# Kernel optimization log

Measured on AMD Instinct MI355X. Metric: run time of the kernel, lower is better.

## Reference

```python
import jax, jax.numpy as jnp
import numpy as np

N, E, G = 50000, 1600000, 64
N_SPECIES, D_ATTR, D, N_RBF = 16, 16, 32, 8
CUTOFF = 5.0
SCALE, SHIFT = 1.0, 0.0


def setup_inputs() -> dict:
    key = jax.random.key(0)
    ks = jax.random.split(key, 20)

    def w(k, shape):
        fan_in = shape[-2] if len(shape) > 1 else shape[-1]
        return jax.random.normal(k, shape, dtype=jnp.float32) / np.sqrt(fan_in)

    return {
        "x": jax.random.randint(ks[0], (N, 1), 0, N_SPECIES),
        "pos": 3.0 * jax.random.normal(ks[1], (N, 3), dtype=jnp.float32),
        "edge_index": jax.random.randint(ks[2], (2, E), 0, N),
        "period_vec": 0.1 * jax.random.normal(ks[3], (E, 3), dtype=jnp.float32),
        "batch": jnp.sort(jax.random.randint(ks[4], (N,), 0, G)),
        "W_elem": w(ks[5], (N_SPECIES, D_ATTR)),
        "W0": w(ks[6], (D_ATTR, D)),
        "b0": jnp.zeros((D,), jnp.float32),
        "Wr1": w(ks[7], (3, N_RBF, D)),
        "br1": jnp.zeros((3, D), jnp.float32),
        "Wr2": w(ks[8], (3, D, D)),
        "Wmsg": w(ks[9], (3, D, D)),
        "Wattr": w(ks[10], (3, D_ATTR, D)),
        "Wself": w(ks[11], (3, D, D)),
        "bconv": jnp.zeros((3, D), jnp.float32),
        "wsh": w(ks[12], (3, 4)),
        "Wp1": w(ks[13], (D, 16)),
        "bp1": jnp.zeros((16,), jnp.float32),
        "Wp2": w(ks[14], (16, 1)),
        "bp2": jnp.zeros((1,), jnp.float32),
    }


def reference(x, pos, edge_index, period_vec, batch, W_elem, W0, b0, Wr1, br1,
              Wr2, Wmsg, Wattr, Wself, bconv, wsh, Wp1, bp1, Wp2, bp2):
    src, dst = edge_index[0], edge_index[1]

    # node_attr_layer: species embedding (gather), then first_atom_embed linear
    x_attr = W_elem[x[:, 0]]                              # [N, D_ATTR]
    h = x_attr @ W0 + b0                                  # [N, D]

    # edge_attr_layer: PBC edge vectors, lengths, l<=1 spherical harmonics
    edge_vec = pos[dst] - pos[src] + period_vec           # [E, 3]
    edge_len = jnp.linalg.norm(edge_vec, axis=-1, keepdims=True)  # [E, 1]
    unit = edge_vec / (edge_len + 1e-9)
    edge_sh = jnp.concatenate([jnp.ones_like(edge_len), unit], axis=-1)  # [E, 4]

    # edge_embedding_layer: Gaussian radial basis of edge lengths
    centers = jnp.linspace(0.0, CUTOFF, N_RBF, dtype=pos.dtype)
    gamma = jnp.asarray((N_RBF / CUTOFF) ** 2, pos.dtype)
    rbf = jnp.exp(-gamma * (edge_len - centers) ** 2)     # [E, N_RBF]

    # 3 conv layers: gather -> per-edge transform -> scatter-sum -> node update
    for i in range(3):
        rw = jax.nn.relu(rbf @ Wr1[i] + br1[i]) @ Wr2[i]  # [E, D] radial MLP
        sh_w = edge_sh @ wsh[i]                           # [E] sh mixing
        msg = (h[src] @ Wmsg[i]) * rw * sh_w[:, None]     # [E, D]
        agg = jax.ops.segment_sum(msg, dst, num_segments=N)  # [N, D]
        h = jax.nn.silu(agg + x_attr @ Wattr[i] + h @ Wself[i] + bconv[i])

    # post_conv layers
    h = jax.nn.silu(h @ Wp1 + bp1)                        # [N, 16]
    h = (h @ Wp2 + bp2)[:, 0]                             # [N] (squeeze)

    # scatter-sum pooling over graphs + affine energy scaling
    e = jax.ops.segment_sum(h, batch, num_segments=G)     # [G]
    return (e * SCALE + SHIFT)[:, None]                   # [G, 1]
```

## Files before the change

### kernel.cpp

```cpp
#include <hip/hip_runtime.h>
#include <hip/hip_fp16.h>
#include <math.h>

constexpr int N_NODES  = 50000;
constexpr int N_EDGES  = 1600000;
constexpr int G_GRAPHS = 64;
constexpr int D        = 32;
constexpr int D_ATTR   = 16;
constexpr int N_RBF    = 8;

constexpr int   TBL      = 8192;
constexpr int   TBL_ROWS = TBL + 1;
constexpr float LMAX     = 10.0f;

constexpr int BUCKET = 80;

constexpr int NT     = 64;
constexpr int NTILES = (N_NODES + NT - 1) / NT;
constexpr int TCAP   = 2432;
constexpr int STHREADS = 512;
constexpr int NBLK1    = 1024;
constexpr int EPB      = (N_EDGES + NBLK1 - 1) / NBLK1;
constexpr int EPV      = (EPB + STHREADS - 1) / STHREADS;

constexpr int NSLOT = NTILES * NT * BUCKET;

typedef unsigned int  uint4v  __attribute__((ext_vector_type(4)));
typedef unsigned int  uint2v  __attribute__((ext_vector_type(2)));

__device__ __forceinline__ float silu(float x) {
    return x / (1.0f + __expf(-x));
}
__device__ __forceinline__ float h2f_bits(unsigned short u) {
    return __half2float(__ushort_as_half(u));
}
__device__ __forceinline__ __half2 h2u(unsigned v) {
    union { unsigned u; __half2 h; } c; c.u = v; return c.h;
}

__device__ __forceinline__ void accum8(uint4v t, uint4v m, float sw, float (&acc)[8]) {
    float2 p0 = __half22float2(__hmul2(h2u(t.x), h2u(m.x)));
    float2 p1 = __half22float2(__hmul2(h2u(t.y), h2u(m.y)));
    float2 p2 = __half22float2(__hmul2(h2u(t.z), h2u(m.z)));
    float2 p3 = __half22float2(__hmul2(h2u(t.w), h2u(m.w)));
    acc[0] = fmaf(p0.x, sw, acc[0]); acc[1] = fmaf(p0.y, sw, acc[1]);
    acc[2] = fmaf(p1.x, sw, acc[2]); acc[3] = fmaf(p1.y, sw, acc[3]);
    acc[4] = fmaf(p2.x, sw, acc[4]); acc[5] = fmaf(p2.y, sw, acc[5]);
    acc[6] = fmaf(p3.x, sw, acc[6]); acc[7] = fmaf(p3.y, sw, acc[7]);
}

__global__ void node_init_kernel(const int* __restrict__ x,
                                 const float* __restrict__ W_elem,
                                 const float* __restrict__ W0,
                                 const float* __restrict__ b0,
                                 const float* __restrict__ Wmsg0,
                                 const float* __restrict__ Wself0,
                                 const float* __restrict__ Wattr,
                                 const float* __restrict__ bconv,
                                 __half* __restrict__ hm0,
                                 float* __restrict__ hs0,
                                 float* __restrict__ xa1,
                                 float* __restrict__ xa2,
                                 float* __restrict__ out) {
    int t = blockIdx.x * blockDim.x + threadIdx.x;
    if (t < G_GRAPHS) out[t] = 0.0f;
    int n = t >> 5, c = t & 31;
    if (n >= N_NODES) return;
    int sp = x[n];
    const float* we = W_elem + sp * D_ATTR;
    float xv = (c < D_ATTR) ? we[c] : 0.0f;
    float acc = b0[c];
#pragma unroll
    for (int a = 0; a < D_ATTR; ++a) acc += we[a] * W0[a * D + c];
    float m = 0.0f, s = 0.0f;
#pragma unroll
    for (int j = 0; j < D; ++j) {
        float hj = __shfl(acc, j, 32);
        m = fmaf(hj, Wmsg0[j * D + c], m);
        s = fmaf(hj, Wself0[j * D + c], s);
    }
    float a0 = bconv[0 * D + c], a1 = bconv[1 * D + c], a2 = bconv[2 * D + c];
#pragma unroll
    for (int j = 0; j < D_ATTR; ++j) {
        float xj = __shfl(xv, j, 32);
        a0 = fmaf(xj, Wattr[0 * D_ATTR * D + j * D + c], a0);
        a1 = fmaf(xj, Wattr[1 * D_ATTR * D + j * D + c], a1);
        a2 = fmaf(xj, Wattr[2 * D_ATTR * D + j * D + c], a2);
    }
    hm0[n * D + c] = __float2half(m);
    hs0[n * D + c] = s + a0;
    xa1[n * D + c] = a1;
    xa2[n * D + c] = a2;
}

__global__ __launch_bounds__(STHREADS, 8) void hist_kernel(const int* __restrict__ eidx,
                                                           int* __restrict__ blk_hist) {
    __shared__ int hist[NTILES];
    int tid = threadIdx.x;
    int e0 = blockIdx.x * EPB;
    int elim = e0 + EPB < N_EDGES ? e0 + EPB : N_EDGES;
    for (int i = tid; i < NTILES; i += STHREADS) hist[i] = 0;
    __syncthreads();
#pragma unroll
    for (int i = 0; i < EPV; ++i) {
        int e = e0 + tid + STHREADS * i;
        if (e < elim) atomicAdd(&hist[eidx[N_EDGES + e] >> 6], 1);
    }
    __syncthreads();
    int* dst = blk_hist + (size_t)blockIdx.x * NTILES;
    for (int t = tid; t < NTILES; t += STHREADS) dst[t] = hist[t];
}

__global__ void scan_kernel(const int* __restrict__ blk_hist,
                            int* __restrict__ blk_base,
                            int* __restrict__ tile_total) {
    int t = blockIdx.x;
    int lane = threadIdx.x;
    int run = 0;
    for (int b0 = 0; b0 < NBLK1; b0 += 64) {
        int b = b0 + lane;
        int v = (b < NBLK1) ? blk_hist[(size_t)b * NTILES + t] : 0;
        int pre = v;
#pragma unroll
        for (int o = 1; o < 64; o <<= 1) {
            int w = __shfl_up(pre, o);
            if (lane >= o) pre += w;
        }
        int excl = pre - v;
        if (b < NBLK1) blk_base[(size_t)b * NTILES + t] = run + excl;
        run += __shfl(pre, 63);
    }
    if (lane == 0) tile_total[t] = run;
}

__global__ __launch_bounds__(STHREADS, 8) void scatter_kernel(const int* __restrict__ eidx,
                                                              const float* __restrict__ pos,
                                                              const float* __restrict__ period,
                                                              const float* __restrict__ wsh,
                                                              const int* __restrict__ blk_base,
                                                              uint4v* __restrict__ bins) {
    __shared__ int hist[NTILES];
    __shared__ int basev[NTILES];
    int tid = threadIdx.x;
    int e0 = blockIdx.x * EPB;
    int elim = e0 + EPB < N_EDGES ? e0 + EPB : N_EDGES;
    const int* bb = blk_base + (size_t)blockIdx.x * NTILES;
    for (int i = tid; i < NTILES; i += STHREADS) {
        hist[i] = 0;
        basev[i] = bb[i];
    }
    __syncthreads();

    int   sarr[EPV], darr[EPV];
    float vx[EPV], vy[EPV], vz[EPV];
#pragma unroll
    for (int i = 0; i < EPV; ++i) {
        int e  = e0 + tid + STHREADS * i;
        int ec = (e < elim) ? e : (elim - 1);
        int s = eidx[ec];
        int d = eidx[N_EDGES + ec];
        sarr[i] = s;
        darr[i] = d;
        vx[i] = pos[d * 3 + 0] - pos[s * 3 + 0] + period[ec * 3 + 0];
        vy[i] = pos[d * 3 + 1] - pos[s * 3 + 1] + period[ec * 3 + 1];
        vz[i] = pos[d * 3 + 2] - pos[s * 3 + 2] + period[ec * 3 + 2];
    }
    asm volatile("" ::
        "v"(vx[0]), "v"(vx[1]), "v"(vx[2]), "v"(vx[3]),
        "v"(vy[0]), "v"(vy[1]), "v"(vy[2]), "v"(vy[3]),
        "v"(vz[0]), "v"(vz[1]), "v"(vz[2]), "v"(vz[3]),
        "v"(sarr[0]), "v"(sarr[1]), "v"(sarr[2]), "v"(sarr[3]),
        "v"(darr[0]), "v"(darr[1]), "v"(darr[2]), "v"(darr[3]));
#pragma unroll
    for (int i = 0; i < EPV; ++i) {
        int e = e0 + tid + STHREADS * i;
        if (e >= elim) continue;
        float len = sqrtf(vx[i] * vx[i] + vy[i] * vy[i] + vz[i] * vz[i]);
        float inv = 1.0f / (len + 1e-9f);
        int idx = (int)fminf(len * ((float)TBL / LMAX) + 0.5f, (float)TBL);
        float sw[3];
#pragma unroll
        for (int l = 0; l < 3; ++l)
            sw[l] = wsh[l * 4 + 0] +
                    (vx[i] * wsh[l * 4 + 1] + vy[i] * wsh[l * 4 + 2] + vz[i] * wsh[l * 4 + 3]) * inv;
        int tile = darr[i] >> 6;
        int rank = atomicAdd(&hist[tile], 1);
        int slot = basev[tile] + rank;
        if (slot < TCAP) {
            unsigned u0 = (unsigned)__half_as_ushort(__float2half(sw[0]));
            unsigned u1 = (unsigned)__half_as_ushort(__float2half(sw[1]));
            unsigned u2 = (unsigned)__half_as_ushort(__float2half(sw[2]));
            uint4v r;
            r.x = (unsigned)sarr[i] | ((unsigned)idx << 16);
            r.y = (unsigned)(darr[i] & (NT - 1));
            r.z = u0 | (u1 << 16);
            r.w = u2;
            bins[(size_t)tile * TCAP + slot] = r;
        }
    }
}

__global__ __launch_bounds__(512, 8) void shuffle_kernel(const uint4v* __restrict__ bins,
                                                         const int* __restrict__ tile_total,
                                                         unsigned int* __restrict__ xs,
                                                         unsigned short* __restrict__ swp,
                                                         int* __restrict__ count) {
    __shared__ int lcur[NT];
    int tile = blockIdx.x;
    int tid = threadIdx.x;
    if (tid < NT) lcur[tid] = 0;
    __syncthreads();
    int cnt = tile_total[tile];
    if (cnt > TCAP) cnt = TCAP;
    const uint4v* base = bins + (size_t)tile * TCAP;
    for (int i = tid; i < cnt; i += 512) {
        uint4v r = __builtin_nontemporal_load(base + i);
        int dl = (int)(r.y & 63u);
        int slot = atomicAdd(&lcur[dl], 1);
        if (slot < BUCKET) {
            size_t g = (size_t)(tile * NT + dl) * BUCKET + slot;
            xs[g] = r.x;
            swp[0 * (size_t)NSLOT + g] = (unsigned short)(r.z & 0xFFFFu);
            swp[1 * (size_t)NSLOT + g] = (unsigned short)(r.z >> 16);
            swp[2 * (size_t)NSLOT + g] = (unsigned short)(r.w & 0xFFFFu);
        }
    }
    __syncthreads();
    if (tid < NT) {
        int node = tile * NT + tid;
        if (node < N_NODES) {
            int c = lcur[tid];
            count[node] = c < BUCKET ? c : BUCKET;
        }
    }
}

__global__ void table_kernel(const float* __restrict__ Wr1,
                             const float* __restrict__ br1,
                             const float* __restrict__ Wr2,
                             __half* __restrict__ table) {
    int t = blockIdx.x * blockDim.x + threadIdx.x;
    if (t >= 3 * TBL_ROWS) return;
    int l = t / TBL_ROWS;
    int idx = t % TBL_ROWS;
    float len = (float)idx * (LMAX / (float)TBL);
    const float gamma = (8.0f / 5.0f) * (8.0f / 5.0f);
    float rbf[N_RBF];
#pragma unroll
    for (int k = 0; k < N_RBF; ++k) {
        float dd = len - (float)k * (5.0f / 7.0f);
        rbf[k] = __expf(-gamma * dd * dd);
    }
    float out[D];
#pragma unroll
    for (int c = 0; c < D; ++c) out[c] = 0.0f;
    for (int j = 0; j < D; ++j) {
        float z = br1[l * D + j];
#pragma unroll
        for (int k = 0; k < N_RBF; ++k) z += rbf[k] * Wr1[l * N_RBF * D + k * D + j];
        z = fmaxf(z, 0.0f);
        const float* w2 = Wr2 + l * D * D + j * D;
#pragma unroll
        for (int c = 0; c < D; ++c) out[c] += z * w2[c];
    }
    __half* dst = table + ((size_t)(l * TBL_ROWS + idx)) * D;
#pragma unroll
    for (int c = 0; c < D; ++c) dst[c] = __float2half(out[c]);
}

template <int LAYER, bool NEXT>
__global__ __launch_bounds__(256, 8) void conv_kernel(const __half* __restrict__ hm,
                            const float* __restrict__ hs,
                            const unsigned int* __restrict__ xs,
                            const unsigned short* __restrict__ swp,
                            const int* __restrict__ count,
                            const __half* __restrict__ table,
                            const float* __restrict__ Wmsg_next,
                            const float* __restrict__ Wself_next,
                            const float* __restrict__ xa_next,
                            __half* __restrict__ hm_out,
                            float* __restrict__ hs_out,
                            float* __restrict__ h_final) {
    __shared__ float sagg[4][2][32];
    int wid = (blockIdx.x * blockDim.x + threadIdx.x) >> 6;
    int na = wid * 2;
    if (na >= N_NODES) return;
    int nb = na + 1;
    int lane = threadIdx.x & 63;
    int w  = (threadIdx.x >> 6) & 3;
    int rg = lane >> 2;
    int cg = lane & 3;

    const uint4v* tab4 = (const uint4v*)(table + (size_t)LAYER * TBL_ROWS * D);
    const uint4v* hm4  = (const uint4v*)hm;
    const unsigned short* swb = swp + (size_t)LAYER * NSLOT;

    int cnta = count[na], cntb = count[nb];
    int bega = na * BUCKET, begb = nb * BUCKET;
    int mx = cnta > cntb ? cnta : cntb;

    float acca[8], accb[8];
#pragma unroll
    for (int j = 0; j < 8; ++j) { acca[j] = 0.0f; accb[j] = 0.0f; }

    for (int k = 0; k < BUCKET; k += 32) {
        int r0 = k + rg, r1 = k + 16 + rg;
        bool va0 = r0 < cnta, va1 = r1 < cnta;
        bool vb0 = r0 < cntb, vb1 = r1 < cntb;
        unsigned ua0 = va0 ? xs[bega + r0] : 0u;
        unsigned ua1 = va1 ? xs[bega + r1] : 0u;
        unsigned ub0 = vb0 ? xs[begb + r0] : 0u;
        unsigned ub1 = vb1 ? xs[begb + r1] : 0u;
        float sa0 = va0 ? h2f_bits(swb[bega + r0]) : 0.0f;
        float sa1 = va1 ? h2f_bits(swb[bega + r1]) : 0.0f;
        float sb0 = vb0 ? h2f_bits(swb[begb + r0]) : 0.0f;
        float sb1 = vb1 ? h2f_bits(swb[begb + r1]) : 0.0f;
        uint4v ta0 = tab4[(size_t)(ua0 >> 16) * 4 + cg];
        uint4v ma0 = hm4[(size_t)(ua0 & 0xFFFFu) * 4 + cg];
        uint4v ta1 = tab4[(size_t)(ua1 >> 16) * 4 + cg];
        uint4v ma1 = hm4[(size_t)(ua1 & 0xFFFFu) * 4 + cg];
        uint4v tb0 = tab4[(size_t)(ub0 >> 16) * 4 + cg];
        uint4v mb0 = hm4[(size_t)(ub0 & 0xFFFFu) * 4 + cg];
        uint4v tb1 = tab4[(size_t)(ub1 >> 16) * 4 + cg];
        uint4v mb1 = hm4[(size_t)(ub1 & 0xFFFFu) * 4 + cg];
        asm volatile("" :: "v"(ta0.x), "v"(ma0.x), "v"(ta1.x), "v"(ma1.x),
                           "v"(tb0.x), "v"(mb0.x), "v"(tb1.x), "v"(mb1.x));
        accum8(ta0, ma0, sa0, acca);
        accum8(ta1, ma1, sa1, acca);
        accum8(tb0, mb0, sb0, accb);
        accum8(tb1, mb1, sb1, accb);
        if (k + 32 >= mx) break;
    }

#pragma unroll
    for (int j = 0; j < 8; ++j) {
        acca[j] += __shfl_xor(acca[j], 4);
        acca[j] += __shfl_xor(acca[j], 8);
        acca[j] += __shfl_xor(acca[j], 16);
        acca[j] += __shfl_xor(acca[j], 32);
        accb[j] += __shfl_xor(accb[j], 4);
        accb[j] += __shfl_xor(accb[j], 8);
        accb[j] += __shfl_xor(accb[j], 16);
        accb[j] += __shfl_xor(accb[j], 32);
    }
    if (rg == 0) {
#pragma unroll
        for (int j = 0; j < 8; ++j) {
            sagg[w][0][cg * 8 + j] = acca[j];
            sagg[w][1][cg * 8 + j] = accb[j];
        }
    }
    __syncthreads();

    int c = lane & 31;
    int hi = lane >> 5;
    int mynode = hi ? nb : na;
    float agg = sagg[w][hi][c];

    float hn = silu(agg + hs[mynode * D + c]);
    if (NEXT) {
        float m = 0.0f, s2 = 0.0f;
#pragma unroll
        for (int j = 0; j < D; ++j) {
            float hj = __shfl(hn, j, 32);
            m  = fmaf(hj, Wmsg_next[j * D + c], m);
            s2 = fmaf(hj, Wself_next[j * D + c], s2);
        }
        hm_out[mynode * D + c] = __float2half(m);
        hs_out[mynode * D + c] = s2 + xa_next[mynode * D + c];
    } else {
        h_final[mynode * D + c] = hn;
    }
}

__global__ void readout_kernel(const float* __restrict__ h,
                               const int* __restrict__ batch,
                               const float* __restrict__ Wp1,
                               const float* __restrict__ bp1,
                               const float* __restrict__ Wp2,
                               const float* __restrict__ bp2,
                               float* __restrict__ out) {
    int n = blockIdx.x * blockDim.x + threadIdx.x;
    float s = 0.0f;
    int b = -1;
    if (n < N_NODES) {
        b = batch[n];
        const float* hrow = h + n * D;
        float acc2 = bp2[0];
#pragma unroll
        for (int m = 0; m < 16; ++m) {
            float a = bp1[m];
#pragma unroll
            for (int j = 0; j < D; ++j) a += hrow[j] * Wp1[j * 16 + m];
            acc2 += silu(a) * Wp2[m];
        }
        s = acc2;
    }
    unsigned long long valid = __ballot(n < N_NODES);
    if (valid == 0ull) return;
    int firstLane = __ffsll(valid) - 1;
    int b0v = __shfl(b, firstLane);
    bool ok = (b == b0v) || (n >= N_NODES);
    if (__all(ok)) {
#pragma unroll
        for (int o = 32; o > 0; o >>= 1) s += __shfl_down(s, o);
        if ((threadIdx.x & 63) == 0) atomicAdd(out + b0v, s);
    } else {
        if (n < N_NODES) atomicAdd(out + b, s);
    }
}

extern "C" void kernel_launch(void* const* d_in, const int* in_sizes, int n_in,
                              void* d_out, int out_size, void* d_ws, size_t ws_size,
                              hipStream_t stream) {
    const int*   x      = (const int*)d_in[0];
    const float* pos    = (const float*)d_in[1];
    const int*   eidx   = (const int*)d_in[2];
    const float* period = (const float*)d_in[3];
    const int*   batch  = (const int*)d_in[4];
    const float* W_elem = (const float*)d_in[5];
    const float* W0     = (const float*)d_in[6];
    const float* b0     = (const float*)d_in[7];
    const float* Wr1    = (const float*)d_in[8];
    const float* br1    = (const float*)d_in[9];
    const float* Wr2    = (const float*)d_in[10];
    const float* Wmsg   = (const float*)d_in[11];
    const float* Wattr  = (const float*)d_in[12];
    const float* Wself  = (const float*)d_in[13];
    const float* bconv  = (const float*)d_in[14];
    const float* wsh    = (const float*)d_in[15];
    const float* Wp1    = (const float*)d_in[16];
    const float* bp1    = (const float*)d_in[17];
    const float* Wp2    = (const float*)d_in[18];
    const float* bp2    = (const float*)d_in[19];

    char* base = (char*)d_ws;
    size_t off = 0;
    auto carve = [&](size_t bytes) -> void* {
        void* p = base + off;
        off = (off + bytes + 255) & ~(size_t)255;
        return p;
    };
    __half*         hm_a        = (__half*)carve((size_t)N_NODES * D * 2);
    __half*         hm_b        = (__half*)carve((size_t)N_NODES * D * 2);
    float*          hs_a        = (float*)carve((size_t)N_NODES * D * 4);
    float*          hs_b        = (float*)carve((size_t)N_NODES * D * 4);
    float*          xa1         = (float*)carve((size_t)N_NODES * D * 4);
    float*          xa2         = (float*)carve((size_t)N_NODES * D * 4);
    float*          h_final     = (float*)carve((size_t)N_NODES * D * 4);
    unsigned int*   xs          = (unsigned int*)carve((size_t)NSLOT * 4);
    unsigned short* swp         = (unsigned short*)carve((size_t)3 * NSLOT * 2);
    uint4v*         bins        = (uint4v*)carve((size_t)NTILES * TCAP * 16);
    int*            blk_hist    = (int*)carve((size_t)NBLK1 * NTILES * 4);
    int*            blk_base    = (int*)carve((size_t)NBLK1 * NTILES * 4);
    int*            tile_total  = (int*)carve((size_t)NTILES * 4);
    int*            count       = (int*)carve((size_t)NTILES * NT * 4);
    __half*         table       = (__half*)carve((size_t)3 * TBL_ROWS * D * 2);
    (void)ws_size; (void)in_sizes; (void)n_in; (void)out_size;

    node_init_kernel<<<(N_NODES * 32 + 255) / 256, 256, 0, stream>>>(
        x, W_elem, W0, b0, Wmsg + 0 * D * D, Wself + 0 * D * D, Wattr, bconv,
        hm_a, hs_a, xa1, xa2, (float*)d_out);
    hist_kernel<<<NBLK1, STHREADS, 0, stream>>>(eidx, blk_hist);
    scan_kernel<<<NTILES, 64, 0, stream>>>(blk_hist, blk_base, tile_total);
    scatter_kernel<<<NBLK1, STHREADS, 0, stream>>>(eidx, pos, period, wsh, blk_base, bins);
    table_kernel<<<(3 * TBL_ROWS + 127) / 128, 128, 0, stream>>>(Wr1, br1, Wr2, table);
    shuffle_kernel<<<NTILES, 512, 0, stream>>>(bins, tile_total, xs, swp, count);

    int cwaves = (N_NODES + 1) / 2;
    int cgrid  = (cwaves * 64 + 255) / 256;
    conv_kernel<0, true><<<cgrid, 256, 0, stream>>>(
        hm_a, hs_a, xs, swp, count, table, Wmsg + 1 * D * D, Wself + 1 * D * D, xa1,
        hm_b, hs_b, nullptr);
    conv_kernel<1, true><<<cgrid, 256, 0, stream>>>(
        hm_b, hs_b, xs, swp, count, table, Wmsg + 2 * D * D, Wself + 2 * D * D, xa2,
        hm_a, hs_a, nullptr);
    conv_kernel<2, false><<<cgrid, 256, 0, stream>>>(
        hm_a, hs_a, xs, swp, count, table, nullptr, nullptr, nullptr,
        nullptr, nullptr, h_final);

    readout_kernel<<<(N_NODES + 255) / 256, 256, 0, stream>>>(h_final, batch, Wp1, bp1, Wp2, bp2,
                                                              (float*)d_out);
}
```

Baseline: 375.3 us.

## Replace tile histogram/scan/shuffle binning with per-node global atomic cursors

Edge bucketing by destination is simplified: instead of a block histogram, a scan, a scatter into tile bins and a shuffle pass, each edge claims a slot in its destination node's fixed bucket with a global atomicAdd on a per-node cursor and writes its packed record there directly. The cursor array is zeroed in the node init kernel and reused as the count, clamped to BUCKET in the conv kernel. This removes three kernels and an intermediate bins buffer, but trades them for contended global atomics and scattered small writes whose slot order is nondeterministic, so the fp summation order varies between runs.

```diff
diff --git a/kernel.cpp b/kernel.cpp
--- a/kernel.cpp
+++ b/kernel.cpp
@@ -14,16 +14,14 @@
 constexpr float LMAX     = 10.0f;
 
 constexpr int BUCKET = 80;
-
 constexpr int NT     = 64;
-constexpr int NTILES = (N_NODES + NT - 1) / NT;
-constexpr int TCAP   = 2432;
+
 constexpr int STHREADS = 512;
 constexpr int NBLK1    = 1024;
 constexpr int EPB      = (N_EDGES + NBLK1 - 1) / NBLK1;
 constexpr int EPV      = (EPB + STHREADS - 1) / STHREADS;
 
-constexpr int NSLOT = NTILES * NT * BUCKET;
+constexpr int NSLOT = N_NODES * BUCKET;
 
 typedef unsigned int  uint4v  __attribute__((ext_vector_type(4)));
 typedef unsigned int  uint2v  __attribute__((ext_vector_type(2)));
@@ -61,9 +59,11 @@
                                  float* __restrict__ hs0,
                                  float* __restrict__ xa1,
                                  float* __restrict__ xa2,
+                                 int* __restrict__ node_cursor,
                                  float* __restrict__ out) {
     int t = blockIdx.x * blockDim.x + threadIdx.x;
     if (t < G_GRAPHS) out[t] = 0.0f;
+    if (t < N_NODES) node_cursor[t] = 0;
     int n = t >> 5, c = t & 31;
     if (n >= N_NODES) return;
     int sp = x[n];
@@ -93,63 +93,16 @@
     xa2[n * D + c] = a2;
 }
 
-__global__ __launch_bounds__(STHREADS, 8) void hist_kernel(const int* __restrict__ eidx,
-                                                           int* __restrict__ blk_hist) {
-    __shared__ int hist[NTILES];
-    int tid = threadIdx.x;
-    int e0 = blockIdx.x * EPB;
-    int elim = e0 + EPB < N_EDGES ? e0 + EPB : N_EDGES;
-    for (int i = tid; i < NTILES; i += STHREADS) hist[i] = 0;
-    __syncthreads();
-#pragma unroll
-    for (int i = 0; i < EPV; ++i) {
-        int e = e0 + tid + STHREADS * i;
-        if (e < elim) atomicAdd(&hist[eidx[N_EDGES + e] >> 6], 1);
-    }
-    __syncthreads();
-    int* dst = blk_hist + (size_t)blockIdx.x * NTILES;
-    for (int t = tid; t < NTILES; t += STHREADS) dst[t] = hist[t];
-}
-
-__global__ void scan_kernel(const int* __restrict__ blk_hist,
-                            int* __restrict__ blk_base,
-                            int* __restrict__ tile_total) {
-    int t = blockIdx.x;
-    int lane = threadIdx.x;
-    int run = 0;
-    for (int b0 = 0; b0 < NBLK1; b0 += 64) {
-        int b = b0 + lane;
-        int v = (b < NBLK1) ? blk_hist[(size_t)b * NTILES + t] : 0;
-        int pre = v;
-#pragma unroll
-        for (int o = 1; o < 64; o <<= 1) {
-            int w = __shfl_up(pre, o);
-            if (lane >= o) pre += w;
-        }
-        int excl = pre - v;
-        if (b < NBLK1) blk_base[(size_t)b * NTILES + t] = run + excl;
-        run += __shfl(pre, 63);
-    }
-    if (lane == 0) tile_total[t] = run;
-}
-
 __global__ __launch_bounds__(STHREADS, 8) void scatter_kernel(const int* __restrict__ eidx,
                                                               const float* __restrict__ pos,
                                                               const float* __restrict__ period,
                                                               const float* __restrict__ wsh,
-                                                              const int* __restrict__ blk_base,
-                                                              uint4v* __restrict__ bins) {
-    __shared__ int hist[NTILES];
-    __shared__ int basev[NTILES];
+                                                              int* __restrict__ node_cursor,
+                                                              unsigned int* __restrict__ xs,
+                                                              unsigned short* __restrict__ swp) {
     int tid = threadIdx.x;
     int e0 = blockIdx.x * EPB;
     int elim = e0 + EPB < N_EDGES ? e0 + EPB : N_EDGES;
-    const int* bb = blk_base + (size_t)blockIdx.x * NTILES;
-    for (int i = tid; i < NTILES; i += STHREADS) {
-        hist[i] = 0;
-        basev[i] = bb[i];
-    }
-    __syncthreads();
 
     int   sarr[EPV], darr[EPV];
     float vx[EPV], vy[EPV], vz[EPV];
@@ -171,10 +124,19 @@
         "v"(vz[0]), "v"(vz[1]), "v"(vz[2]), "v"(vz[3]),
         "v"(sarr[0]), "v"(sarr[1]), "v"(sarr[2]), "v"(sarr[3]),
         "v"(darr[0]), "v"(darr[1]), "v"(darr[2]), "v"(darr[3]));
+
+    int slot[EPV];
 #pragma unroll
     for (int i = 0; i < EPV; ++i) {
         int e = e0 + tid + STHREADS * i;
-        if (e >= elim) continue;
+        slot[i] = (e < elim) ? atomicAdd(&node_cursor[darr[i]], 1) : BUCKET;
+    }
+    asm volatile("" :: "v"(slot[0]), "v"(slot[1]), "v"(slot[2]), "v"(slot[3]));
+
+#pragma unroll
+    for (int i = 0; i < EPV; ++i) {
+        int e = e0 + tid + STHREADS * i;
+        if (e >= elim || slot[i] >= BUCKET) continue;
         float len = sqrtf(vx[i] * vx[i] + vy[i] * vy[i] + vz[i] * vz[i]);
         float inv = 1.0f / (len + 1e-9f);
         int idx = (int)fminf(len * ((float)TBL / LMAX) + 0.5f, (float)TBL);
@@ -183,55 +145,11 @@
         for (int l = 0; l < 3; ++l)
             sw[l] = wsh[l * 4 + 0] +
                     (vx[i] * wsh[l * 4 + 1] + vy[i] * wsh[l * 4 + 2] + vz[i] * wsh[l * 4 + 3]) * inv;
-        int tile = darr[i] >> 6;
-        int rank = atomicAdd(&hist[tile], 1);
-        int slot = basev[tile] + rank;
-        if (slot < TCAP) {
-            unsigned u0 = (unsigned)__half_as_ushort(__float2half(sw[0]));
-            unsigned u1 = (unsigned)__half_as_ushort(__float2half(sw[1]));
-            unsigned u2 = (unsigned)__half_as_ushort(__float2half(sw[2]));
-            uint4v r;
-            r.x = (unsigned)sarr[i] | ((unsigned)idx << 16);
-            r.y = (unsigned)(darr[i] & (NT - 1));
-            r.z = u0 | (u1 << 16);
-            r.w = u2;
-            bins[(size_t)tile * TCAP + slot] = r;
-        }
-    }
-}
-
-__global__ __launch_bounds__(512, 8) void shuffle_kernel(const uint4v* __restrict__ bins,
-                                                         const int* __restrict__ tile_total,
-                                                         unsigned int* __restrict__ xs,
-                                                         unsigned short* __restrict__ swp,
-                                                         int* __restrict__ count) {
-    __shared__ int lcur[NT];
-    int tile = blockIdx.x;
-    int tid = threadIdx.x;
-    if (tid < NT) lcur[tid] = 0;
-    __syncthreads();
-    int cnt = tile_total[tile];
-    if (cnt > TCAP) cnt = TCAP;
-    const uint4v* base = bins + (size_t)tile * TCAP;
-    for (int i = tid; i < cnt; i += 512) {
-        uint4v r = __builtin_nontemporal_load(base + i);
-        int dl = (int)(r.y & 63u);
-        int slot = atomicAdd(&lcur[dl], 1);
-        if (slot < BUCKET) {
-            size_t g = (size_t)(tile * NT + dl) * BUCKET + slot;
-            xs[g] = r.x;
-            swp[0 * (size_t)NSLOT + g] = (unsigned short)(r.z & 0xFFFFu);
-            swp[1 * (size_t)NSLOT + g] = (unsigned short)(r.z >> 16);
-            swp[2 * (size_t)NSLOT + g] = (unsigned short)(r.w & 0xFFFFu);
-        }
-    }
-    __syncthreads();
-    if (tid < NT) {
-        int node = tile * NT + tid;
-        if (node < N_NODES) {
-            int c = lcur[tid];
-            count[node] = c < BUCKET ? c : BUCKET;
-        }
+        size_t g = (size_t)darr[i] * BUCKET + slot[i];
+        xs[g] = (unsigned)sarr[i] | ((unsigned)idx << 16);
+        swp[0 * (size_t)NSLOT + g] = __half_as_ushort(__float2half(sw[0]));
+        swp[1 * (size_t)NSLOT + g] = __half_as_ushort(__float2half(sw[1]));
+        swp[2 * (size_t)NSLOT + g] = __half_as_ushort(__float2half(sw[2]));
     }
 }
 
@@ -295,7 +213,8 @@
     const uint4v* hm4  = (const uint4v*)hm;
     const unsigned short* swb = swp + (size_t)LAYER * NSLOT;
 
-    int cnta = count[na], cntb = count[nb];
+    int cnta = count[na]; cnta = cnta < BUCKET ? cnta : BUCKET;
+    int cntb = count[nb]; cntb = cntb < BUCKET ? cntb : BUCKET;
     int bega = na * BUCKET, begb = nb * BUCKET;
     int mx = cnta > cntb ? cnta : cntb;
 
@@ -450,33 +369,27 @@
     float*          h_final     = (float*)carve((size_t)N_NODES * D * 4);
     unsigned int*   xs          = (unsigned int*)carve((size_t)NSLOT * 4);
     unsigned short* swp         = (unsigned short*)carve((size_t)3 * NSLOT * 2);
-    uint4v*         bins        = (uint4v*)carve((size_t)NTILES * TCAP * 16);
-    int*            blk_hist    = (int*)carve((size_t)NBLK1 * NTILES * 4);
-    int*            blk_base    = (int*)carve((size_t)NBLK1 * NTILES * 4);
-    int*            tile_total  = (int*)carve((size_t)NTILES * 4);
-    int*            count       = (int*)carve((size_t)NTILES * NT * 4);
+    int*            node_cursor = (int*)carve((size_t)N_NODES * 4);
     __half*         table       = (__half*)carve((size_t)3 * TBL_ROWS * D * 2);
     (void)ws_size; (void)in_sizes; (void)n_in; (void)out_size;
 
     node_init_kernel<<<(N_NODES * 32 + 255) / 256, 256, 0, stream>>>(
         x, W_elem, W0, b0, Wmsg + 0 * D * D, Wself + 0 * D * D, Wattr, bconv,
-        hm_a, hs_a, xa1, xa2, (float*)d_out);
-    hist_kernel<<<NBLK1, STHREADS, 0, stream>>>(eidx, blk_hist);
-    scan_kernel<<<NTILES, 64, 0, stream>>>(blk_hist, blk_base, tile_total);
-    scatter_kernel<<<NBLK1, STHREADS, 0, stream>>>(eidx, pos, period, wsh, blk_base, bins);
+        hm_a, hs_a, xa1, xa2, node_cursor, (float*)d_out);
+    scatter_kernel<<<NBLK1, STHREADS, 0, stream>>>(eidx, pos, period, wsh,
+                                                   node_cursor, xs, swp);
     table_kernel<<<(3 * TBL_ROWS + 127) / 128, 128, 0, stream>>>(Wr1, br1, Wr2, table);
-    shuffle_kernel<<<NTILES, 512, 0, stream>>>(bins, tile_total, xs, swp, count);
 
     int cwaves = (N_NODES + 1) / 2;
     int cgrid  = (cwaves * 64 + 255) / 256;
     conv_kernel<0, true><<<cgrid, 256, 0, stream>>>(
-        hm_a, hs_a, xs, swp, count, table, Wmsg + 1 * D * D, Wself + 1 * D * D, xa1,
+        hm_a, hs_a, xs, swp, node_cursor, table, Wmsg + 1 * D * D, Wself + 1 * D * D, xa1,
         hm_b, hs_b, nullptr);
     conv_kernel<1, true><<<cgrid, 256, 0, stream>>>(
-        hm_b, hs_b, xs, swp, count, table, Wmsg + 2 * D * D, Wself + 2 * D * D, xa2,
+        hm_b, hs_b, xs, swp, node_cursor, table, Wmsg + 2 * D * D, Wself + 2 * D * D, xa2,
         hm_a, hs_a, nullptr);
     conv_kernel<2, false><<<cgrid, 256, 0, stream>>>(
-        hm_a, hs_a, xs, swp, count, table, nullptr, nullptr, nullptr,
+        hm_a, hs_a, xs, swp, node_cursor, table, nullptr, nullptr, nullptr,
         nullptr, nullptr, h_final);
 
     readout_kernel<<<(N_NODES + 255) / 256, 256, 0, stream>>>(h_final, batch, Wp1, bp1, Wp2, bp2,
```

Result: slower. 408.5 us (+8.9%).
